# Performance work log

Measured on AMD Instinct MI355X. Metric: run time of the kernel, lower is better.

Reference implementation:

```python
import jax, jax.numpy as jnp
import numpy as np

D_MODEL = 1024
N_HEADS = 16
N_LAYERS = 4
N_LEVELS = 8
B, T = 2, 1024
EPS = 1e-5
ADALN_K = 0.1
ADALN_C = 2.0
FMAX = float(np.finfo(np.float32).max)


def setup_inputs() -> dict:
    key = jax.random.key(0)
    ks = jax.random.split(key, 12)
    d, L = D_MODEL, N_LAYERS
    x = jax.random.normal(ks[0], (B, T, d), dtype=jnp.float32)
    # ragged lengths -> padding mask (1 valid, 0 pad), shape (b, t, 1)
    lengths = jnp.array([T, (3 * T) // 4], dtype=jnp.int32)
    m = (jnp.arange(T)[None, :] < lengths[:, None]).astype(jnp.float32)[..., None]
    l = jax.random.randint(ks[1], (B,), 0, N_LEVELS, dtype=jnp.int32)
    s = 0.02
    Wqkv = jax.random.normal(ks[2], (L, d, 3 * d), dtype=jnp.float32) * s
    Wout = jax.random.normal(ks[3], (L, d, d), dtype=jnp.float32) * s
    bout = jnp.zeros((L, d), dtype=jnp.float32)
    adaln_attn = jax.random.normal(ks[4], (L, N_LEVELS, 2 * d), dtype=jnp.float32) * s
    adaln_ffn = jax.random.normal(ks[5], (L, N_LEVELS, 2 * d), dtype=jnp.float32) * s
    W1 = jax.random.normal(ks[6], (L, d, 4 * d), dtype=jnp.float32) * s
    b1 = jnp.zeros((L, 4 * d), dtype=jnp.float32)
    W2 = jax.random.normal(ks[7], (L, 4 * d, d), dtype=jnp.float32) * s
    b2 = jnp.zeros((L, d), dtype=jnp.float32)
    return dict(x=x, m=m, l=l, Wqkv=Wqkv, Wout=Wout, bout=bout,
                adaln_attn=adaln_attn, adaln_ffn=adaln_ffn,
                W1=W1, b1=b1, W2=W2, b2=b2)


def _adaln(x, emb, l):
    # emb: (n_levels, 2d); l: (b,)
    g = emb[l][:, None, :]                      # (b, 1, 2d)
    loggamma, beta = jnp.split(g, 2, axis=-1)
    mu = jnp.mean(x, axis=-1, keepdims=True)
    var = jnp.mean((x - mu) ** 2, axis=-1, keepdims=True)
    h = (x - mu) * jax.lax.rsqrt(var + EPS)
    h = ADALN_C * (1.0 - jax.lax.stop_gradient(ADALN_K * h)) * h
    return jnp.exp(loggamma) * h + beta


def _attention(x, m, Wqkv, Wout, bout):
    b, t, d = x.shape
    h = N_HEADS
    dh = d // h
    qkv = x @ Wqkv                               # (b, t, 3d)
    q, k, v = jnp.split(qkv, 3, axis=-1)
    q = q.reshape(b, t, h, dh)
    k = k.reshape(b, t, h, dh)
    v = v.reshape(b, t, h, dh)
    e = jnp.einsum('bihd,bjhd->bijh', q, k) * (dh ** -0.5)
    kpm = m[:, None, :, :] * m[:, :, None, :]    # (b, i, j, 1)
    causal = jnp.tril(jnp.ones((t, t), dtype=kpm.dtype))[None, :, :, None]
    kpm = kpm * causal
    e = jnp.where(kpm == 0, -FMAX, e)
    a = jax.nn.softmax(e, axis=2)                # softmax over j (dim=2), matches custom softmax
    o = jnp.einsum('bijh,bjhd->bihd', a, v).reshape(b, t, d)
    o = o @ Wout + bout
    return o * m


def reference(x, m, l, Wqkv, Wout, bout, adaln_attn, adaln_ffn, W1, b1, W2, b2):
    for i in range(N_LAYERS):
        # attention sub-block (PrenormResidual with AdaLN, requires_mask=True)
        h = _adaln(x, adaln_attn[i], l) * m
        x = (x + _attention(h, m, Wqkv[i], Wout[i], bout[i])) * m
        # FFN sub-block
        h = _adaln(x, adaln_ffn[i], l) * m
        ff = jax.nn.gelu(h @ W1[i] + b1[i], approximate=False) @ W2[i] + b2[i]
        x = (x + ff) * m
    return x
```

## Files before the change

kernel.cpp:

```cpp
#include <hip/hip_runtime.h>

#define D_MODEL 1024
#define N_HEADS 16
#define DH 64
#define N_LAYERS 4
#define N_LEVELS 8
#define BB 2
#define TT 1024
#define MM (BB*TT)
#define EPSV 1e-5f

typedef float f32x4 __attribute__((ext_vector_type(4)));
typedef short bf16x8 __attribute__((ext_vector_type(8)));
typedef unsigned short u16x4 __attribute__((ext_vector_type(4)));

__device__ __forceinline__ float bf2f(unsigned short u) {
    union { unsigned int i; float f; } c; c.i = ((unsigned int)u) << 16; return c.f;
}
__device__ __forceinline__ unsigned short f2bf(float f) {
    union { float f; unsigned int i; } c; c.f = f;
    unsigned int x = c.i;
    return (unsigned short)((x + 0x7fffu + ((x >> 16) & 1u)) >> 16);
}
__device__ __forceinline__ float cvt_in(const void* src, long long j, int isbf) {
    return isbf ? bf2f(((const unsigned short*)src)[j]) : ((const float*)src)[j];
}

__device__ __forceinline__ void gl_lds16(const unsigned short* g, unsigned short* l) {
    __builtin_amdgcn_global_load_lds(
        (const __attribute__((address_space(1))) unsigned int*)g,
        (__attribute__((address_space(3))) unsigned int*)l,
        16, 0, 0);
}

template<int N> __device__ __forceinline__ void wait_vm() {
    asm volatile("s_waitcnt vmcnt(%0)" :: "i"(N) : "memory");
}

__global__ void detect_kernel(const unsigned short* __restrict__ x, int* __restrict__ flag) {
    __shared__ int cnts[256];
    int cnt = 0;
    for (int i = threadIdx.x; i < 16384; i += 256) {
        unsigned short u = x[2 * i];
        int e = (u >> 7) & 0xFF;
        if (e >= 110 && e <= 140) cnt++;
    }
    cnts[threadIdx.x] = cnt;
    __syncthreads();
    for (int s = 128; s; s >>= 1) {
        if (threadIdx.x < s) cnts[threadIdx.x] += cnts[threadIdx.x + s];
        __syncthreads();
    }
    if (threadIdx.x == 0) flag[0] = (cnts[0] > 12000) ? 1 : 0;
}

__global__ void load_f32_kernel(const void* __restrict__ src, float* __restrict__ dst,
                                const int* __restrict__ flag, int n) {
    int i = blockIdx.x * 256 + threadIdx.x;
    if (i >= n) return;
    dst[i] = cvt_in(src, i, flag[0]);
}
__global__ void load_small_kernel(const void* m_in, const void* aa, const void* af_,
                                  const void* bo, const void* b1, const void* b2,
                                  float* mf, float* embA, float* embF,
                                  float* boutf, float* b1f, float* b2f,
                                  const int* __restrict__ flag) {
    int i = blockIdx.x * 256 + threadIdx.x;
    int isbf = flag[0];
    if (i < 2048)        mf[i] = cvt_in(m_in, i, isbf);
    else if (i < 67584)  embA[i - 2048] = cvt_in(aa, i - 2048, isbf);
    else if (i < 133120) embF[i - 67584] = cvt_in(af_, i - 67584, isbf);
    else if (i < 137216) boutf[i - 133120] = cvt_in(bo, i - 133120, isbf);
    else if (i < 153600) b1f[i - 137216] = cvt_in(b1, i - 137216, isbf);
    else if (i < 157696) b2f[i - 153600] = cvt_in(b2, i - 153600, isbf);
}

__global__ __launch_bounds__(256)
void transpose_layer_kernel(const void* Wqkv, const void* Wo, const void* W1, const void* W2,
                            unsigned short* wq, unsigned short* wo,
                            unsigned short* w1, unsigned short* w2,
                            const int* __restrict__ flag,
                            long long o_qkv, long long o_o, long long o_1, long long o_2) {
    __shared__ float tile[32][33];
    int bid = blockIdx.x;
    const void* src; unsigned short* dst; long long off; int N, K, nt, kt;
    if (bid < 3072)      { int t = bid;        src = Wqkv; dst = wq; off = o_qkv; N = 3072; K = 1024; nt = t % 96;  kt = t / 96; }
    else if (bid < 4096) { int t = bid - 3072; src = Wo;   dst = wo; off = o_o;   N = 1024; K = 1024; nt = t % 32;  kt = t / 32; }
    else if (bid < 8192) { int t = bid - 4096; src = W1;   dst = w1; off = o_1;   N = 4096; K = 1024; nt = t % 128; kt = t / 128; }
    else                 { int t = bid - 8192; src = W2;   dst = w2; off = o_2;   N = 1024; K = 4096; nt = t % 32;  kt = t / 32; }
    int n0 = nt * 32, k0 = kt * 32;
    int r = threadIdx.x >> 5, c = threadIdx.x & 31;
    int isbf = flag[0];
    #pragma unroll
    for (int rr = 0; rr < 4; ++rr) {
        int k = k0 + r + rr * 8;
        tile[r + rr * 8][c] = cvt_in(src, off + (long long)k * N + n0 + c, isbf);
    }
    __syncthreads();
    #pragma unroll
    for (int rr = 0; rr < 4; ++rr) {
        int n = n0 + r + rr * 8;
        dst[(size_t)n * K + k0 + c] = f2bf(tile[c][r + rr * 8]);
    }
}

__device__ __forceinline__ void blk_sum2_256(float& a, float& b, float* red) {
    #pragma unroll
    for (int off = 32; off; off >>= 1) {
        a += __shfl_down(a, off, 64);
        b += __shfl_down(b, off, 64);
    }
    int tid = threadIdx.x;
    __syncthreads();
    if ((tid & 63) == 0) { red[tid >> 6] = a; red[4 + (tid >> 6)] = b; }
    __syncthreads();
    a = red[0] + red[1] + red[2] + red[3];
    b = red[4] + red[5] + red[6] + red[7];
}

__global__ __launch_bounds__(256)
void adaln_kernel(const float* __restrict__ x,
                  const float* __restrict__ emb,
                  const int* __restrict__ lvl,
                  const float* __restrict__ mvec,
                  unsigned short* __restrict__ h) {
    __shared__ float red[8];
    int row = blockIdx.x;
    int b = row / TT;
    int tid = threadIdx.x;
    const float* xr = x + (size_t)row * D_MODEL;
    float mval = mvec[row];
    unsigned short* hr = h + (size_t)row * D_MODEL;

    if (mval == 0.0f) {
        u16x4 z = (u16x4)0;
        *(u16x4*)(hr + 4 * tid) = z;
        return;
    }

    f32x4 xv = *(const f32x4*)(xr + 4 * tid);
    float s = xv[0] + xv[1] + xv[2] + xv[3];
    float ss = xv[0]*xv[0] + xv[1]*xv[1] + xv[2]*xv[2] + xv[3]*xv[3];
    blk_sum2_256(s, ss, red);
    float mu = s * (1.0f / D_MODEL);
    float var = ss * (1.0f / D_MODEL) - mu * mu;
    float rstd = rsqrtf(var + EPSV);

    int lv = lvl[b];
    const float* g = emb + (size_t)lv * (2 * D_MODEL);
    f32x4 lg = *(const f32x4*)(g + 4 * tid);
    f32x4 lb = *(const f32x4*)(g + D_MODEL + 4 * tid);
    u16x4 r;
    #pragma unroll
    for (int c = 0; c < 4; ++c) {
        float hn = (xv[c] - mu) * rstd;
        float h2 = 2.0f * (1.0f - 0.1f * hn) * hn;
        float o = __expf(lg[c]) * h2 + lb[c];
        r[c] = f2bf(o * mval);
    }
    *(u16x4*)(hr + 4 * tid) = r;
}

#define EPI_STORE 0
#define EPI_GELU  1
#define EPI_RESID 2
#define EPI_PART  3

template<int MI, int NI, int WR, int WC>
__global__ __launch_bounds__(WR * WC * 64)
void gemm8_kernel(const unsigned short* __restrict__ A, int lda,
                  const unsigned short* __restrict__ BT, int ldb,
                  const float* __restrict__ bias,
                  unsigned short* __restrict__ outb,
                  const float* __restrict__ xin,
                  float* __restrict__ xout,
                  const float* __restrict__ mvec,
                  float* __restrict__ pbuf,
                  int M, int N, int K, int mode) {
    constexpr int BM = WR * MI * 16;
    constexpr int BN = WC * NI * 16;
    constexpr int NW = WR * WC;
    constexpr int NSA = BM / 16;
    constexpr int NSB = BN / 16;
    static_assert(NSA % NW == 0, "A staging must divide evenly over waves");
    constexpr int LA  = NSA / NW;
    constexpr int LB0 = NSB / NW;
    constexpr int LBr = NSB % NW;
    __shared__ __align__(16) unsigned short As[4][BM * 32];
    __shared__ __align__(16) unsigned short Bs[4][BN * 32];
    __shared__ int alive;
    int tid = threadIdx.x;
    int wave = tid >> 6;
    int lane = tid & 63;
    int quad = lane >> 4;
    int l16  = lane & 15;
    int tileM = blockIdx.y * BM;
    int tileN = blockIdx.x * BN;
    int wm = (wave % WR) * MI * 16;
    int wn = (wave / WR) * NI * 16;

    if (tid == 0) alive = 0;
    __syncthreads();
    if (tid < BM && mvec[tileM + tid] != 0.0f) alive = 1;
    __syncthreads();

    f32x4 acc[MI][NI] = {};

    if (alive) {
        long long zoff = (long long)blockIdx.z * K;
        const unsigned short* Ab = A  + zoff + (size_t)(tileM + (lane >> 2)) * lda + (lane & 3) * 8;
        const unsigned short* Bb = BT + zoff + (size_t)(tileN + (lane >> 2)) * ldb + (lane & 3) * 8;

        auto stage = [&](int t, int buf) {
            int k0 = t * 32;
            #pragma unroll
            for (int st = wave, i = 0; i < LA; st += NW, ++i)
                gl_lds16(Ab + (size_t)st * 16 * lda + k0, &As[buf][st * 512]);
            for (int st = wave; st < NSB; st += NW)
                gl_lds16(Bb + (size_t)st * 16 * ldb + k0, &Bs[buf][st * 512]);
        };
        auto compute = [&](int buf) {
            __builtin_amdgcn_sched_barrier(0);
            bf16x8 af[MI], bf[NI];
            #pragma unroll
            for (int mi = 0; mi < MI; ++mi)
                af[mi] = *(const bf16x8*)(&As[buf][(wm + mi * 16 + l16) * 32 + quad * 8]);
            #pragma unroll
            for (int ni = 0; ni < NI; ++ni)
                bf[ni] = *(const bf16x8*)(&Bs[buf][(wn + ni * 16 + l16) * 32 + quad * 8]);
            #pragma unroll
            for (int mi = 0; mi < MI; ++mi)
                #pragma unroll
                for (int ni = 0; ni < NI; ++ni)
                    acc[mi][ni] = __builtin_amdgcn_mfma_f32_16x16x32_bf16(af[mi], bf[ni], acc[mi][ni], 0, 0, 0);
        };

        int nt = K / 32;
        stage(0, 0);
        stage(1, 1);
        for (int t = 0; t + 2 < nt; ++t) {
            stage(t + 2, (t + 2) & 3);
            if (LBr && wave < LBr) wait_vm<2 * (LA + LB0 + 1)>();
            else                   wait_vm<2 * (LA + LB0)>();
            __builtin_amdgcn_s_barrier();
            compute(t & 3);
        }
        {
            if (LBr && wave < LBr) wait_vm<LA + LB0 + 1>();
            else                   wait_vm<LA + LB0>();
            __builtin_amdgcn_s_barrier();
            compute((nt - 2) & 3);
        }
        {
            wait_vm<0>();
            __builtin_amdgcn_s_barrier();
            compute((nt - 1) & 3);
        }
    }

    #pragma unroll
    for (int mi = 0; mi < MI; ++mi)
    #pragma unroll
    for (int ni = 0; ni < NI; ++ni) {
        #pragma unroll
        for (int r = 0; r < 4; ++r) {
            int row = tileM + wm + mi * 16 + quad * 4 + r;
            int col = tileN + wn + ni * 16 + l16;
            float v = acc[mi][ni][r];
            size_t idx = (size_t)row * N + col;
            if (mode == EPI_STORE) {
                outb[idx] = f2bf(v);
            } else if (mode == EPI_GELU) {
                v += bias[col];
                float gel = 0.5f * v * (1.0f + erff(v * 0.70710678118654752f));
                outb[idx] = f2bf(gel);
            } else if (mode == EPI_RESID) {
                v += bias[col];
                xout[idx] = (xin[idx] + v) * mvec[row];
            } else {
                pbuf[(size_t)blockIdx.z * M * N + idx] = v;
            }
        }
    }
}

#define FA_DPAD 72

__global__ __launch_bounds__(256)
void fattn_split_kernel(const unsigned short* __restrict__ qkv,
                        const float* __restrict__ mvec,
                        float* __restrict__ Opart,
                        float* __restrict__ ml) {
    __shared__ __align__(16) unsigned short Qs[64 * FA_DPAD];
    __shared__ __align__(16) unsigned short Ks[64 * FA_DPAD];
    __shared__ __align__(16) unsigned short Vs[64 * FA_DPAD];
    __shared__ __align__(16) unsigned short Ps[64 * FA_DPAD];
    __shared__ int alive_s;

    int qt  = blockIdx.x;
    int hd  = blockIdx.y;
    int b   = blockIdx.z >> 1;
    int s   = blockIdx.z & 1;
    int tid = threadIdx.x;
    int wave = tid >> 6;
    int lane = tid & 63;
    int quad = lane >> 4;
    int l16  = lane & 15;

    if (tid == 0) alive_s = 0;
    __syncthreads();
    if (tid < 64 && mvec[(size_t)b * TT + qt * 64 + tid] != 0.0f) alive_s = 1;
    __syncthreads();
    bool alive = alive_s != 0;

    const unsigned short* base = qkv + (size_t)b * TT * 3072;

    f32x4 Oacc[4] = {};
    float mstate[4], lstate[4];
    #pragma unroll
    for (int r = 0; r < 4; ++r) {
        mstate[r] = alive ? -1e30f : 0.f;
        lstate[r] = alive ? 0.f : 1.f;
    }

    if (alive) {
        {
            int r = tid >> 2, c = (tid & 3) * 16;
            const unsigned short* src = base + (size_t)(qt * 64 + r) * 3072 + hd * DH + c;
            *(uint4*)(&Qs[r * FA_DPAD + c])     = *(const uint4*)(src);
            *(uint4*)(&Qs[r * FA_DPAD + c + 8]) = *(const uint4*)(src + 8);
        }
        __syncthreads();

        bf16x8 aq[2];
        #pragma unroll
        for (int cc = 0; cc < 2; ++cc)
            aq[cc] = *(const bf16x8*)(&Qs[(wave * 16 + l16) * FA_DPAD + cc * 32 + quad * 8]);

        for (int jt = s; jt <= qt; jt += 2) {
            __syncthreads();
            {
                int r = tid >> 2, c = (tid & 3) * 16;
                const unsigned short* src = base + (size_t)(jt * 64 + r) * 3072 + 1024 + hd * DH + c;
                *(uint4*)(&Ks[r * FA_DPAD + c])     = *(const uint4*)(src);
                *(uint4*)(&Ks[r * FA_DPAD + c + 8]) = *(const uint4*)(src + 8);
            }
            {
                int j = lane, c = wave * 16;
                const unsigned short* src = base + (size_t)(jt * 64 + j) * 3072 + 2048 + hd * DH + c;
                unsigned short tmp[16];
                *(uint4*)(tmp)     = *(const uint4*)(src);
                *(uint4*)(tmp + 8) = *(const uint4*)(src + 8);
                #pragma unroll
                for (int d = 0; d < 16; ++d) Vs[(c + d) * FA_DPAD + j] = tmp[d];
            }
            __syncthreads();

            f32x4 S[4] = {};
            #pragma unroll
            for (int t = 0; t < 4; ++t)
                #pragma unroll
                for (int cc = 0; cc < 2; ++cc) {
                    bf16x8 bk = *(const bf16x8*)(&Ks[(t * 16 + l16) * FA_DPAD + cc * 32 + quad * 8]);
                    S[t] = __builtin_amdgcn_mfma_f32_16x16x32_bf16(aq[cc], bk, S[t], 0, 0, 0);
                }

            int qrow0 = qt * 64 + wave * 16 + quad * 4;
            bool diag = (jt == qt);
            float mnew[4];
            #pragma unroll
            for (int r = 0; r < 4; ++r) {
                float v = -1e30f;
                #pragma unroll
                for (int t = 0; t < 4; ++t) {
                    float sv = S[t][r] * 0.125f;
                    if (diag) {
                        int j = jt * 64 + t * 16 + l16;
                        if (j > qrow0 + r) sv = -1e30f;
                    }
                    S[t][r] = sv;
                    v = fmaxf(v, sv);
                }
                v = fmaxf(v, __shfl_xor(v, 1, 64));
                v = fmaxf(v, __shfl_xor(v, 2, 64));
                v = fmaxf(v, __shfl_xor(v, 4, 64));
                v = fmaxf(v, __shfl_xor(v, 8, 64));
                mnew[r] = fmaxf(mstate[r], v);
            }

            #pragma unroll
            for (int r = 0; r < 4; ++r) {
                float rs = 0.f;
                #pragma unroll
                for (int t = 0; t < 4; ++t) {
                    float p = __expf(S[t][r] - mnew[r]);
                    rs += p;
                    Ps[(wave * 16 + quad * 4 + r) * FA_DPAD + t * 16 + l16] = f2bf(p);
                }
                rs += __shfl_xor(rs, 1, 64);
                rs += __shfl_xor(rs, 2, 64);
                rs += __shfl_xor(rs, 4, 64);
                rs += __shfl_xor(rs, 8, 64);
                float alpha = __expf(mstate[r] - mnew[r]);
                lstate[r] = alpha * lstate[r] + rs;
                mstate[r] = mnew[r];
                #pragma unroll
                for (int t = 0; t < 4; ++t) Oacc[t][r] *= alpha;
            }

            #pragma unroll
            for (int cc = 0; cc < 2; ++cc) {
                bf16x8 ap = *(const bf16x8*)(&Ps[(wave * 16 + l16) * FA_DPAD + cc * 32 + quad * 8]);
                #pragma unroll
                for (int t = 0; t < 4; ++t) {
                    bf16x8 bv = *(const bf16x8*)(&Vs[(t * 16 + l16) * FA_DPAD + cc * 32 + quad * 8]);
                    Oacc[t] = __builtin_amdgcn_mfma_f32_16x16x32_bf16(ap, bv, Oacc[t], 0, 0, 0);
                }
            }
        }
    }

    #pragma unroll
    for (int r = 0; r < 4; ++r) {
        int qi = qt * 64 + wave * 16 + quad * 4 + r;
        size_t row = (size_t)b * TT + qi;
        float* orow = Opart + (size_t)s * MM * D_MODEL + row * D_MODEL + hd * DH;
        #pragma unroll
        for (int t = 0; t < 4; ++t)
            orow[t * 16 + l16] = Oacc[t][r];
        if (l16 == 0) {
            float* mlp = ml + (((size_t)s * MM + row) * N_HEADS + hd) * 2;
            mlp[0] = mstate[r];
            mlp[1] = lstate[r];
        }
    }
}

__global__ void attn_merge_kernel(const float* __restrict__ Opart,
                                  const float* __restrict__ ml,
                                  unsigned short* __restrict__ ob) {
    int i = blockIdx.x * 256 + threadIdx.x;
    int row = i >> 10;
    int hd  = (i >> 6) & 15;
    const float* ml0 = ml + (((size_t)row) * N_HEADS + hd) * 2;
    const float* ml1 = ml + (((size_t)MM + row) * N_HEADS + hd) * 2;
    float m0 = ml0[0], l0 = ml0[1];
    float m1 = ml1[0], l1 = ml1[1];
    float M = fmaxf(m0, m1);
    float w0 = __expf(m0 - M), w1 = __expf(m1 - M);
    float den = w0 * l0 + w1 * l1;
    float num = w0 * Opart[i] + w1 * Opart[(size_t)MM * D_MODEL + i];
    ob[i] = f2bf(num / den);
}

__global__ void combine2_kernel(float* __restrict__ xf,
                                const float* __restrict__ pbuf,
                                const float* __restrict__ bias,
                                const float* __restrict__ mvec,
                                void* __restrict__ outp,
                                const int* __restrict__ flag, int n) {
    int i = blockIdx.x * 256 + threadIdx.x;
    if (i >= n) return;
    int row = i >> 10, col = i & 1023;
    float v = (xf[i] + pbuf[i] + pbuf[n + i] + bias[col]) * mvec[row];
    xf[i] = v;
    if (outp) {
        if (flag[0]) ((unsigned short*)outp)[i] = f2bf(v);
        else         ((float*)outp)[i] = v;
    }
}

#define MB (1048576u)
#define WS_FLAG   0u
#define WS_MF     4096u
#define WS_EMBA   (WS_MF + 8192u)
#define WS_EMBF   (WS_EMBA + 262144u)
#define WS_BOUT   (WS_EMBF + 262144u)
#define WS_B1     (WS_BOUT + 16384u)
#define WS_B2     (WS_B1 + 65536u)
#define WS_XF     (1u*MB)
#define WS_H      (9u*MB)
#define WS_QKV    (13u*MB)
#define WS_OB     (25u*MB)
#define WS_PART   (9u*MB)
#define WS_ML     (9u*MB)
#define WS_FF1    (29u*MB)
#define WS_OPART  (29u*MB)
#define WS_WQKV   (45u*MB)
#define WS_WOUT   (51u*MB)
#define WS_W1     (53u*MB)
#define WS_W2     (61u*MB)

extern "C" void kernel_launch(void* const* d_in, const int* in_sizes, int n_in,
                              void* d_out, int out_size, void* d_ws, size_t ws_size,
                              hipStream_t stream) {
    const void* x_in  = d_in[0];
    const void* m_in  = d_in[1];
    const int*  l_in  = (const int*)d_in[2];
    const void* Wqkv  = d_in[3];
    const void* Wout  = d_in[4];
    const void* boutp = d_in[5];
    const void* ada_a = d_in[6];
    const void* ada_f = d_in[7];
    const void* W1    = d_in[8];
    const void* b1    = d_in[9];
    const void* W2    = d_in[10];
    const void* b2    = d_in[11];

    char* ws = (char*)d_ws;
    int*            flag = (int*)(ws + WS_FLAG);
    float*          mf   = (float*)(ws + WS_MF);
    float*          embA = (float*)(ws + WS_EMBA);
    float*          embF = (float*)(ws + WS_EMBF);
    float*          boutf= (float*)(ws + WS_BOUT);
    float*          b1f  = (float*)(ws + WS_B1);
    float*          b2f  = (float*)(ws + WS_B2);
    float*          xf   = (float*)(ws + WS_XF);
    unsigned short* h    = (unsigned short*)(ws + WS_H);
    unsigned short* qkv  = (unsigned short*)(ws + WS_QKV);
    unsigned short* ob   = (unsigned short*)(ws + WS_OB);
    float*          part = (float*)(ws + WS_PART);
    float*          mlb  = (float*)(ws + WS_ML);
    float*          opart= (float*)(ws + WS_OPART);
    unsigned short* ff1  = (unsigned short*)(ws + WS_FF1);
    unsigned short* wqkvt= (unsigned short*)(ws + WS_WQKV);
    unsigned short* woutt= (unsigned short*)(ws + WS_WOUT);
    unsigned short* w1t  = (unsigned short*)(ws + WS_W1);
    unsigned short* w2t  = (unsigned short*)(ws + WS_W2);

    const int n = MM * D_MODEL;

    detect_kernel<<<1, 256, 0, stream>>>((const unsigned short*)x_in, flag);
    load_f32_kernel<<<n / 256, 256, 0, stream>>>(x_in, xf, flag, n);
    load_small_kernel<<<(157696 + 255) / 256, 256, 0, stream>>>(
        m_in, ada_a, ada_f, boutp, b1, b2, mf, embA, embF, boutf, b1f, b2f, flag);

    const long long nqkv = (long long)D_MODEL * 3 * D_MODEL;
    const long long nsq  = (long long)D_MODEL * D_MODEL;
    const long long nw1  = (long long)D_MODEL * 4 * D_MODEL;

    for (int i = 0; i < N_LAYERS; ++i) {
        transpose_layer_kernel<<<12288, 256, 0, stream>>>(
            Wqkv, Wout, W1, W2, wqkvt, woutt, w1t, w2t, flag,
            i * nqkv, i * nsq, i * nw1, i * nw1);

        adaln_kernel<<<MM, 256, 0, stream>>>(xf, embA + (size_t)i * N_LEVELS * 2 * D_MODEL, l_in, mf, h);
        gemm8_kernel<4,2,2,2><<<dim3(3072 / 64, MM / 128), 256, 0, stream>>>(
            h, 1024, wqkvt, 1024, nullptr, qkv, nullptr, nullptr, mf, nullptr,
            MM, 3072, 1024, EPI_STORE);
        fattn_split_kernel<<<dim3(TT / 64, N_HEADS, BB * 2), 256, 0, stream>>>(qkv, mf, opart, mlb);
        attn_merge_kernel<<<n / 256, 256, 0, stream>>>(opart, mlb, ob);
        gemm8_kernel<2,2,4,2><<<dim3(1024 / 64, MM / 128), 512, 0, stream>>>(
            ob, 1024, woutt, 1024, boutf + (size_t)i * D_MODEL, nullptr, xf, xf, mf, nullptr,
            MM, 1024, 1024, EPI_RESID);
        adaln_kernel<<<MM, 256, 0, stream>>>(xf, embF + (size_t)i * N_LEVELS * 2 * D_MODEL, l_in, mf, h);
        gemm8_kernel<4,2,2,4><<<dim3(4096 / 128, MM / 128), 512, 0, stream>>>(
            h, 1024, w1t, 1024, b1f + (size_t)i * 4 * D_MODEL, ff1, nullptr, nullptr, mf, nullptr,
            MM, 4096, 1024, EPI_GELU);
        gemm8_kernel<2,2,4,2><<<dim3(1024 / 64, MM / 128, 2), 512, 0, stream>>>(
            ff1, 4096, w2t, 4096, nullptr, nullptr, nullptr, nullptr, mf, part,
            MM, 1024, 2048, EPI_PART);
        combine2_kernel<<<n / 256, 256, 0, stream>>>(
            xf, part, b2f + (size_t)i * D_MODEL, mf,
            (i == N_LAYERS - 1) ? d_out : nullptr, flag, n);
    }
}
```

Before: 938.8 us.

## Swizzle workgroup order, retile GEMMs, use split-K 4, vectorize merge and combine kernels

Remaps the flat workgroup index so that consecutive IDs are spread across the 8 XCDs (round-robin over chiplets) in both the GEMM and flash-attention kernels. MFMA blocks are wrapped in s_setprio to raise wave priority. The QKV and FFN1 GEMMs move to larger 128x128 tiles with 256 threads, and FFN2 goes from split-K 2 to split-K 4 with a matching combine kernel. The merge and combine kernels are vectorized to four elements per thread. The trade-offs are more partial-sum traffic from the extra split, fewer workgroups on the larger tiles, and higher register pressure.

```diff
diff --git a/kernel.cpp b/kernel.cpp
--- a/kernel.cpp
+++ b/kernel.cpp
@@ -194,8 +194,18 @@
     int lane = tid & 63;
     int quad = lane >> 4;
     int l16  = lane & 15;
-    int tileM = blockIdx.y * BM;
-    int tileN = blockIdx.x * BN;
+
+    int gx = gridDim.x, gy = gridDim.y;
+    int nwg = gx * gy * gridDim.z;
+    int fl  = (blockIdx.z * gy + blockIdx.y) * gx + blockIdx.x;
+    int fl2 = (fl & 7) * (nwg >> 3) + (fl >> 3);
+    int bx = fl2 % gx;
+    int rem = fl2 / gx;
+    int by = rem % gy;
+    int bz = rem / gy;
+
+    int tileM = by * BM;
+    int tileN = bx * BN;
     int wm = (wave % WR) * MI * 16;
     int wn = (wave / WR) * NI * 16;
 
@@ -207,7 +217,7 @@
     f32x4 acc[MI][NI] = {};
 
     if (alive) {
-        long long zoff = (long long)blockIdx.z * K;
+        long long zoff = (long long)bz * K;
         const unsigned short* Ab = A  + zoff + (size_t)(tileM + (lane >> 2)) * lda + (lane & 3) * 8;
         const unsigned short* Bb = BT + zoff + (size_t)(tileN + (lane >> 2)) * ldb + (lane & 3) * 8;
 
@@ -228,11 +238,13 @@
             #pragma unroll
             for (int ni = 0; ni < NI; ++ni)
                 bf[ni] = *(const bf16x8*)(&Bs[buf][(wn + ni * 16 + l16) * 32 + quad * 8]);
+            __builtin_amdgcn_s_setprio(1);
             #pragma unroll
             for (int mi = 0; mi < MI; ++mi)
                 #pragma unroll
                 for (int ni = 0; ni < NI; ++ni)
                     acc[mi][ni] = __builtin_amdgcn_mfma_f32_16x16x32_bf16(af[mi], bf[ni], acc[mi][ni], 0, 0, 0);
+            __builtin_amdgcn_s_setprio(0);
         };
 
         int nt = K / 32;
@@ -278,7 +290,7 @@
                 v += bias[col];
                 xout[idx] = (xin[idx] + v) * mvec[row];
             } else {
-                pbuf[(size_t)blockIdx.z * M * N + idx] = v;
+                pbuf[(size_t)bz * M * N + idx] = v;
             }
         }
     }
@@ -297,10 +309,16 @@
     __shared__ __align__(16) unsigned short Ps[64 * FA_DPAD];
     __shared__ int alive_s;
 
-    int qt  = blockIdx.x;
-    int hd  = blockIdx.y;
-    int b   = blockIdx.z >> 1;
-    int s   = blockIdx.z & 1;
+    int gx = gridDim.x, gy = gridDim.y;
+    int nwg = gx * gy * gridDim.z;
+    int fl  = (blockIdx.z * gy + blockIdx.y) * gx + blockIdx.x;
+    int fl2 = (fl & 7) * (nwg >> 3) + (fl >> 3);
+    int qt = fl2 % gx;
+    int rem = fl2 / gx;
+    int hd = rem % gy;
+    int zz = rem / gy;
+    int b   = zz >> 1;
+    int s   = zz & 1;
     int tid = threadIdx.x;
     int wave = tid >> 6;
     int lane = tid & 63;
@@ -439,7 +457,8 @@
 __global__ void attn_merge_kernel(const float* __restrict__ Opart,
                                   const float* __restrict__ ml,
                                   unsigned short* __restrict__ ob) {
-    int i = blockIdx.x * 256 + threadIdx.x;
+    int i4 = blockIdx.x * 256 + threadIdx.x;
+    int i = i4 * 4;
     int row = i >> 10;
     int hd  = (i >> 6) & 15;
     const float* ml0 = ml + (((size_t)row) * N_HEADS + hd) * 2;
@@ -448,25 +467,46 @@
     float m1 = ml1[0], l1 = ml1[1];
     float M = fmaxf(m0, m1);
     float w0 = __expf(m0 - M), w1 = __expf(m1 - M);
-    float den = w0 * l0 + w1 * l1;
-    float num = w0 * Opart[i] + w1 * Opart[(size_t)MM * D_MODEL + i];
-    ob[i] = f2bf(num / den);
-}
-
-__global__ void combine2_kernel(float* __restrict__ xf,
+    float invden = 1.0f / (w0 * l0 + w1 * l1);
+    f32x4 a = *(const f32x4*)(Opart + i);
+    f32x4 c = *(const f32x4*)(Opart + (size_t)MM * D_MODEL + i);
+    u16x4 r;
+    #pragma unroll
+    for (int k = 0; k < 4; ++k) r[k] = f2bf((w0 * a[k] + w1 * c[k]) * invden);
+    *(u16x4*)(ob + i) = r;
+}
+
+__global__ void combine4_kernel(float* __restrict__ xf,
                                 const float* __restrict__ pbuf,
                                 const float* __restrict__ bias,
                                 const float* __restrict__ mvec,
                                 void* __restrict__ outp,
                                 const int* __restrict__ flag, int n) {
-    int i = blockIdx.x * 256 + threadIdx.x;
+    int i4 = blockIdx.x * 256 + threadIdx.x;
+    int i = i4 * 4;
     if (i >= n) return;
     int row = i >> 10, col = i & 1023;
-    float v = (xf[i] + pbuf[i] + pbuf[n + i] + bias[col]) * mvec[row];
-    xf[i] = v;
+    f32x4 x  = *(const f32x4*)(xf + i);
+    f32x4 p0 = *(const f32x4*)(pbuf + i);
+    f32x4 p1 = *(const f32x4*)(pbuf + (size_t)n + i);
+    f32x4 p2 = *(const f32x4*)(pbuf + (size_t)2 * n + i);
+    f32x4 p3 = *(const f32x4*)(pbuf + (size_t)3 * n + i);
+    f32x4 bb = *(const f32x4*)(bias + col);
+    float mv = mvec[row];
+    f32x4 v;
+    #pragma unroll
+    for (int k = 0; k < 4; ++k)
+        v[k] = (x[k] + p0[k] + p1[k] + p2[k] + p3[k] + bb[k]) * mv;
+    *(f32x4*)(xf + i) = v;
     if (outp) {
-        if (flag[0]) ((unsigned short*)outp)[i] = f2bf(v);
-        else         ((float*)outp)[i] = v;
+        if (flag[0]) {
+            u16x4 r;
+            #pragma unroll
+            for (int k = 0; k < 4; ++k) r[k] = f2bf(v[k]);
+            *(u16x4*)((unsigned short*)outp + i) = r;
+        } else {
+            *(f32x4*)((float*)outp + i) = v;
+        }
     }
 }
 
@@ -482,7 +522,6 @@
 #define WS_H      (9u*MB)
 #define WS_QKV    (13u*MB)
 #define WS_OB     (25u*MB)
-#define WS_PART   (9u*MB)
 #define WS_ML     (9u*MB)
 #define WS_FF1    (29u*MB)
 #define WS_OPART  (29u*MB)
@@ -490,6 +529,7 @@
 #define WS_WOUT   (51u*MB)
 #define WS_W1     (53u*MB)
 #define WS_W2     (61u*MB)
+#define WS_PART4  (69u*MB)
 
 extern "C" void kernel_launch(void* const* d_in, const int* in_sizes, int n_in,
                               void* d_out, int out_size, void* d_ws, size_t ws_size,
@@ -519,7 +559,6 @@
     unsigned short* h    = (unsigned short*)(ws + WS_H);
     unsigned short* qkv  = (unsigned short*)(ws + WS_QKV);
     unsigned short* ob   = (unsigned short*)(ws + WS_OB);
-    float*          part = (float*)(ws + WS_PART);
     float*          mlb  = (float*)(ws + WS_ML);
     float*          opart= (float*)(ws + WS_OPART);
     unsigned short* ff1  = (unsigned short*)(ws + WS_FF1);
@@ -527,6 +566,7 @@
     unsigned short* woutt= (unsigned short*)(ws + WS_WOUT);
     unsigned short* w1t  = (unsigned short*)(ws + WS_W1);
     unsigned short* w2t  = (unsigned short*)(ws + WS_W2);
+    float*          part4= (float*)(ws + WS_PART4);
 
     const int n = MM * D_MODEL;
 
@@ -545,23 +585,23 @@
             i * nqkv, i * nsq, i * nw1, i * nw1);
 
         adaln_kernel<<<MM, 256, 0, stream>>>(xf, embA + (size_t)i * N_LEVELS * 2 * D_MODEL, l_in, mf, h);
-        gemm8_kernel<4,2,2,2><<<dim3(3072 / 64, MM / 128), 256, 0, stream>>>(
+        gemm8_kernel<4,4,2,2><<<dim3(3072 / 128, MM / 128), 256, 0, stream>>>(
             h, 1024, wqkvt, 1024, nullptr, qkv, nullptr, nullptr, mf, nullptr,
             MM, 3072, 1024, EPI_STORE);
         fattn_split_kernel<<<dim3(TT / 64, N_HEADS, BB * 2), 256, 0, stream>>>(qkv, mf, opart, mlb);
-        attn_merge_kernel<<<n / 256, 256, 0, stream>>>(opart, mlb, ob);
+        attn_merge_kernel<<<n / 1024, 256, 0, stream>>>(opart, mlb, ob);
         gemm8_kernel<2,2,4,2><<<dim3(1024 / 64, MM / 128), 512, 0, stream>>>(
             ob, 1024, woutt, 1024, boutf + (size_t)i * D_MODEL, nullptr, xf, xf, mf, nullptr,
             MM, 1024, 1024, EPI_RESID);
         adaln_kernel<<<MM, 256, 0, stream>>>(xf, embF + (size_t)i * N_LEVELS * 2 * D_MODEL, l_in, mf, h);
-        gemm8_kernel<4,2,2,4><<<dim3(4096 / 128, MM / 128), 512, 0, stream>>>(
+        gemm8_kernel<4,4,2,2><<<dim3(4096 / 128, MM / 128), 256, 0, stream>>>(
             h, 1024, w1t, 1024, b1f + (size_t)i * 4 * D_MODEL, ff1, nullptr, nullptr, mf, nullptr,
             MM, 4096, 1024, EPI_GELU);
-        gemm8_kernel<2,2,4,2><<<dim3(1024 / 64, MM / 128, 2), 512, 0, stream>>>(
-            ff1, 4096, w2t, 4096, nullptr, nullptr, nullptr, nullptr, mf, part,
-            MM, 1024, 2048, EPI_PART);
-        combine2_kernel<<<n / 256, 256, 0, stream>>>(
-            xf, part, b2f + (size_t)i * D_MODEL, mf,
+        gemm8_kernel<4,4,2,2><<<dim3(1024 / 128, MM / 128, 4), 256, 0, stream>>>(
+            ff1, 4096, w2t, 4096, nullptr, nullptr, nullptr, nullptr, mf, part4,
+            MM, 1024, 1024, EPI_PART);
+        combine4_kernel<<<n / 1024, 256, 0, stream>>>(
+            xf, part4, b2f + (size_t)i * D_MODEL, mf,
             (i == N_LAYERS - 1) ? d_out : nullptr, flag, n);
     }
 }
```

After: 997.4 us. +6.2%, slower.
